# Performance work log

Hardware: AMD Instinct MI355X
Metric: run time of the kernel (lower is better)

The kernel has to match this reference:

```python
import jax, jax.numpy as jnp
import numpy as np

H = 16  # num_heads
THETA = 10000.0


def apply_rope(x, positions, theta=THETA):
    # x: [..., S, d_k]; positions: [S]
    d_k = x.shape[-1]
    inv_freq = theta ** (-jnp.arange(0, d_k, 2, dtype=jnp.float32) / d_k)  # [d_k/2]
    ang = positions.astype(jnp.float32)[:, None] * inv_freq[None, :]  # [S, d_k/2]
    cos, sin = jnp.cos(ang), jnp.sin(ang)
    x1 = x[..., 0::2]
    x2 = x[..., 1::2]
    out_even = x1 * cos - x2 * sin
    out_odd = x1 * sin + x2 * cos
    out = jnp.stack([out_even, out_odd], axis=-1)  # [..., S, d_k/2, 2]
    return out.reshape(x.shape)


def setup_inputs() -> dict:
    key = jax.random.key(0)
    k1, k2, k3 = jax.random.split(key, 3)
    B, S, D = 2, 2048, 1024
    x = jax.random.normal(k1, (B, S, D), dtype=jnp.float32)
    token_positions = jnp.arange(S, dtype=jnp.int32)
    w_qkv = jax.random.normal(k2, (3 * D, D), dtype=jnp.float32) * (D ** -0.5)
    w_out = jax.random.normal(k3, (D, D), dtype=jnp.float32) * (D ** -0.5)
    return {"x": x, "token_positions": token_positions, "w_qkv": w_qkv, "w_out": w_out}


def reference(x, token_positions, w_qkv, w_out):
    B, S, D = x.shape
    d_k = D // H
    qkv = jnp.einsum('bsd,ed->bse', x, w_qkv)  # [B,S,3D]
    # split '(n h d_k)' -> n=3, h=H, d_k
    qkv = qkv.reshape(B, S, 3, H, d_k).transpose(2, 0, 3, 1, 4)  # [3,B,H,S,d_k]
    q = apply_rope(qkv[0], token_positions)
    k = apply_rope(qkv[1], token_positions)
    v = qkv[2]
    scale = 1.0 / jnp.sqrt(jnp.asarray(d_k, dtype=x.dtype))
    scores = jnp.einsum('bhqd,bhkd->bhqk', q, k) * scale  # [B,H,S,S]
    causal = jnp.tril(jnp.ones((S, S), dtype=bool))
    scores = jnp.where(causal, scores, jnp.asarray(-1e30, dtype=scores.dtype))
    attn = jax.nn.softmax(scores, axis=-1)
    out = jnp.einsum('bhqk,bhkd->bhqd', attn, v)  # [B,H,S,d_k]
    out = out.transpose(0, 2, 1, 3).reshape(B, S, D)  # merge (h d_v)
    return jnp.einsum('bsd,ed->bse', out, w_out)
```

## Files before the change

### kernel.cpp

```cpp
#include <hip/hip_runtime.h>

using bf16 = __bf16;
typedef __bf16 bf16x2 __attribute__((ext_vector_type(2)));
typedef __bf16 bf16x4v __attribute__((ext_vector_type(4)));
typedef __bf16 bf16x8 __attribute__((ext_vector_type(8)));
typedef float f32x4 __attribute__((ext_vector_type(4)));
typedef float floatx4 __attribute__((ext_vector_type(4)));

#define MFMA16(a, b, c) __builtin_amdgcn_mfma_f32_16x16x32_bf16((a), (b), (c), 0, 0, 0)

__device__ __forceinline__ float exp2a(float x) {
  float r;
  asm("v_exp_f32 %0, %1" : "=v"(r) : "v"(x));
  return r;
}

__global__ __launch_bounds__(256) void cast3_kernel(const float* __restrict__ a,
                                                    const float* __restrict__ b,
                                                    const float* __restrict__ c,
                                                    bf16* __restrict__ oa,
                                                    bf16* __restrict__ ob,
                                                    bf16* __restrict__ oc,
                                                    const int* __restrict__ pos,
                                                    float2* __restrict__ tab) {
  int i = blockIdx.x * 256 + threadIdx.x;
  if (i < 65536) {
    int s = i >> 5, ip = i & 31;
    float freq = exp2f(-(float)ip * (13.287712379549449f / 32.0f));
    float ang = (float)pos[s] * freq;
    float sn, cs;
    sincosf(ang, &sn, &cs);
    tab[i] = make_float2(cs, sn);
  }
  const float* in;
  bf16* out;
  int off;
  if (i < 1048576) {
    in = a; out = oa; off = i;
  } else if (i < 1835008) {
    in = b; out = ob; off = i - 1048576;
  } else {
    in = c; out = oc; off = i - 1835008;
  }
  floatx4 v = *(const floatx4*)(in + (size_t)off * 4);
  bf16x4v o;
  #pragma unroll
  for (int j = 0; j < 4; ++j) o[j] = (bf16)v[j];
  *(bf16x4v*)(out + (size_t)off * 4) = o;
}

template <bool OUT_F32, bool ROPE>
__global__ __launch_bounds__(256, 2) void gemm_bt(const bf16* __restrict__ A,
                                                  const bf16* __restrict__ B,
                                                  void* __restrict__ Cv,
                                                  int M, int N, int K,
                                                  const float2* __restrict__ tab) {
  __shared__ bf16 As[128 * 32];
  __shared__ bf16 Bs[128 * 32];
  const int t = threadIdx.x;
  const int l = t & 63;
  const int w = t >> 6;
  const int m0 = blockIdx.y * 128;
  const int n0 = blockIdx.x * 128;
  const int wr = (w >> 1) * 64;
  const int wc = (w & 1) * 64;
  const int lr = l & 15;
  const int lk = (l >> 4) * 8;

  f32x4 acc[4][4] = {};

  const int srow = t >> 2;
  const int scol = (t & 3) * 8;

  for (int k0 = 0; k0 < K; k0 += 32) {
    __syncthreads();
    #pragma unroll
    for (int j = 0; j < 2; ++j) {
      const bf16* ga = A + (size_t)(m0 + j * 64 + srow) * K + k0 + scol;
      __builtin_amdgcn_global_load_lds(
          (const __attribute__((address_space(1))) void*)ga,
          (__attribute__((address_space(3))) void*)(As + (j * 64 + srow) * 32 + scol),
          16, 0, 0);
      const bf16* gb = B + (size_t)(n0 + j * 64 + srow) * K + k0 + scol;
      __builtin_amdgcn_global_load_lds(
          (const __attribute__((address_space(1))) void*)gb,
          (__attribute__((address_space(3))) void*)(Bs + (j * 64 + srow) * 32 + scol),
          16, 0, 0);
    }
    __syncthreads();
    bf16x8 af[4], bfr[4];
    #pragma unroll
    for (int i = 0; i < 4; ++i) af[i] = *(const bf16x8*)(As + (wr + i * 16 + lr) * 32 + lk);
    #pragma unroll
    for (int i = 0; i < 4; ++i) bfr[i] = *(const bf16x8*)(Bs + (wc + i * 16 + lr) * 32 + lk);
    #pragma unroll
    for (int i = 0; i < 4; ++i)
      #pragma unroll
      for (int j = 0; j < 4; ++j)
        acc[i][j] = MFMA16(af[i], bfr[j], acc[i][j]);
  }

  const int cr0 = (l >> 4) * 4;
  const int cc = l & 15;

  if constexpr (ROPE) {
    if (n0 < 2048) {
      int ip[4];
      #pragma unroll
      for (int j = 0; j < 4; ++j) ip[j] = ((n0 + wc + j * 16 + cc) & 63) >> 1;
      const float sgn = (cc & 1) ? 1.f : -1.f;
      #pragma unroll
      for (int i = 0; i < 4; ++i) {
        #pragma unroll
        for (int r = 0; r < 4; ++r) {
          int row = m0 + wr + i * 16 + cr0 + r;
          int s = row & 2047;
          #pragma unroll
          for (int j = 0; j < 4; ++j) {
            float2 cs = tab[s * 32 + ip[j]];
            float self = acc[i][j][r];
            float partner = __shfl_xor(self, 1, 64);
            acc[i][j][r] = self * cs.x + sgn * cs.y * partner;
          }
        }
      }
    }
  }

  #pragma unroll
  for (int i = 0; i < 4; ++i) {
    #pragma unroll
    for (int j = 0; j < 4; ++j) {
      int row = m0 + wr + i * 16 + cr0;
      int col = n0 + wc + j * 16 + cc;
      #pragma unroll
      for (int r = 0; r < 4; ++r) {
        if constexpr (OUT_F32)
          ((float*)Cv)[(size_t)(row + r) * N + col] = acc[i][j][r];
        else
          ((bf16*)Cv)[(size_t)(row + r) * N + col] = (bf16)acc[i][j][r];
      }
    }
  }
}

__global__ __launch_bounds__(512, 4) void fa_causal(const bf16* __restrict__ qkv,
                                                    bf16* __restrict__ attn) {
  const int bh = blockIdx.x;
  const int b = bh >> 4, h = bh & 15;
  const int q0 = ((int)gridDim.y - 1 - (int)blockIdx.y) * 128;
  const int t = threadIdx.x, w = t >> 6, l = t & 63;
  const int lq = l & 15;
  const int g = l >> 4;
  const int lk = g * 8;
  const int swz = lq & 7;
  const int hz = lq >> 3;

  __shared__ bf16 SH[4][64 * 64];

  const size_t rs = 3072;
  const bf16* Qg = qkv + (size_t)(b * 2048) * rs + h * 64;
  const bf16* Kg = Qg + 1024;
  const bf16* Vg = Qg + 2048;

  const int qrow0 = q0 + w * 16;
  const int qg = qrow0 + lq;

  const float SC = 0.125f * 1.44269504088896f;
  bf16x8 qfr[2];
  #pragma unroll
  for (int kk = 0; kk < 2; ++kk) {
    bf16x8 qv = *(const bf16x8*)(Qg + (size_t)qg * rs + kk * 32 + lk);
    #pragma unroll
    for (int j = 0; j < 8; ++j) qv[j] = (bf16)((float)qv[j] * SC);
    qfr[kk] = qv;
  }

  f32x4 o[4] = {};
  float mrow = -1e30f, lrow = 0.f;

  const int nkt = (q0 + 128) >> 6;
  const int krow_in = l >> 3;
  const int kcsrc = (l & 7) ^ krow_in;
  const int kp = t >> 4;
  const int K0 = kp * 2;
  const int sub = (t >> 3) & 1;
  const int cd = t & 7;
  const int slot0 = (K0 & 32) | (((K0 >> 2) & 3) << 3) | (((K0 >> 4) & 1) << 2) | (K0 & 3);

  bf16x4v va4, vb4;

  #define STAGE_K(KT, BUF)                                                              \
    {                                                                                   \
      const bf16* src = Kg + (size_t)((KT)*64 + w * 8 + krow_in) * rs + kcsrc * 8;      \
      __builtin_amdgcn_global_load_lds(                                                 \
          (const __attribute__((address_space(1))) void*)src,                           \
          (__attribute__((address_space(3))) void*)(&SH[BUF][(w * 8) * 64]), 16, 0, 0); \
    }
  #define LOAD_V(KT)                                                                   \
    {                                                                                  \
      const bf16* vsrc = Vg + (size_t)((KT)*64 + K0) * rs + cd * 8 + sub * 4;          \
      va4 = *(const bf16x4v*)(vsrc);                                                   \
      vb4 = *(const bf16x4v*)(vsrc + rs);                                              \
    }
  #define WRITE_V(BUF)                                                                 \
    {                                                                                  \
      _Pragma("unroll")                                                                \
      for (int j = 0; j < 4; ++j) {                                                    \
        int e = sub * 4 + j;                                                           \
        bf16x2 pr;                                                                     \
        pr[0] = va4[j];                                                                \
        pr[1] = vb4[j];                                                                \
        *(bf16x2*)(&SH[2 + (BUF)][(cd * 8 + e) * 64 + (slot0 ^ ((e ^ cd) << 3))]) = pr; \
      }                                                                                \
    }

  STAGE_K(0, 0)
  LOAD_V(0)
  WRITE_V(0)
  __syncthreads();

  for (int kt = 0; kt < nkt; ++kt) {
    const bool pf = (kt + 1 < nkt);
    if (pf) {
      LOAD_V(kt + 1)
      STAGE_K(kt + 1, (kt + 1) & 1)
    }

    if (kt * 64 <= qrow0 + 15) {
      const bf16* Kc = SH[kt & 1];
      const bf16* Vc = SH[2 + (kt & 1)];
      const bool fullw = (kt * 64 + 63 <= qrow0);

      f32x4 sc[4] = {};
      __builtin_amdgcn_s_setprio(1);
      #pragma unroll
      for (int kf = 0; kf < 4; ++kf) {
        const int krow = kf * 16 + lq;
        bf16x8 kb0 = *(const bf16x8*)(&Kc[krow * 64 + ((0 + g) ^ swz) * 8]);
        bf16x8 kb1 = *(const bf16x8*)(&Kc[krow * 64 + ((4 + g) ^ swz) * 8]);
        sc[kf] = MFMA16(kb0, qfr[0], sc[kf]);
        sc[kf] = MFMA16(kb1, qfr[1], sc[kf]);
      }
      __builtin_amdgcn_s_setprio(0);

      float pv[16];
      if (fullw) {
        #pragma unroll
        for (int i = 0; i < 16; ++i) pv[i] = sc[i >> 2][i & 3];
      } else {
        #pragma unroll
        for (int kf = 0; kf < 4; ++kf)
          #pragma unroll
          for (int r = 0; r < 4; ++r) {
            int key = kt * 64 + kf * 16 + g * 4 + r;
            pv[kf * 4 + r] = (key <= qg) ? sc[kf][r] : -1e30f;
          }
      }
      float m0_ = fmaxf(pv[0], pv[1]), m1_ = fmaxf(pv[2], pv[3]);
      float m2_ = fmaxf(pv[4], pv[5]), m3_ = fmaxf(pv[6], pv[7]);
      float m4_ = fmaxf(pv[8], pv[9]), m5_ = fmaxf(pv[10], pv[11]);
      float m6_ = fmaxf(pv[12], pv[13]), m7_ = fmaxf(pv[14], pv[15]);
      float ma = fmaxf(fmaxf(m0_, m1_), fmaxf(m2_, m3_));
      float mb = fmaxf(fmaxf(m4_, m5_), fmaxf(m6_, m7_));
      float mxl = fmaxf(ma, mb);
      if (!__all(mxl <= mrow)) {
        float mx = fmaxf(mxl, __shfl_xor(mxl, 16, 64));
        mx = fmaxf(mx, __shfl_xor(mx, 32, 64));
        float mnew = fmaxf(mrow, mx);
        float al = exp2a(mrow - mnew);
        lrow *= al;
        #pragma unroll
        for (int fd = 0; fd < 4; ++fd)
          #pragma unroll
          for (int r = 0; r < 4; ++r) o[fd][r] *= al;
        mrow = mnew;
      }
      #pragma unroll
      for (int i = 0; i < 16; ++i) pv[i] = exp2a(pv[i] - mrow);
      float s0_ = pv[0] + pv[1], s1_ = pv[2] + pv[3];
      float s2_ = pv[4] + pv[5], s3_ = pv[6] + pv[7];
      float s4_ = pv[8] + pv[9], s5_ = pv[10] + pv[11];
      float s6_ = pv[12] + pv[13], s7_ = pv[14] + pv[15];
      float rsum = ((s0_ + s1_) + (s2_ + s3_)) + ((s4_ + s5_) + (s6_ + s7_));
      rsum += __shfl_xor(rsum, 16, 64);
      rsum += __shfl_xor(rsum, 32, 64);
      lrow += rsum;

      bf16x8 p0, p1;
      #pragma unroll
      for (int i = 0; i < 8; ++i) {
        p0[i] = (bf16)pv[i];
        p1[i] = (bf16)pv[8 + i];
      }

      __builtin_amdgcn_s_setprio(1);
      #pragma unroll
      for (int fd = 0; fd < 4; ++fd) {
        const int drow = fd * 16 + lq;
        {
          int pc = (0 * 4 + g) ^ swz ^ (fd << 1) ^ hz;
          bf16x8 vb = *(const bf16x8*)(&Vc[drow * 64 + pc * 8]);
          o[fd] = MFMA16(vb, p0, o[fd]);
        }
        {
          int pc = (1 * 4 + g) ^ swz ^ (fd << 1) ^ hz;
          bf16x8 vb = *(const bf16x8*)(&Vc[drow * 64 + pc * 8]);
          o[fd] = MFMA16(vb, p1, o[fd]);
        }
      }
      __builtin_amdgcn_s_setprio(0);
    }

    if (pf) {
      WRITE_V((kt + 1) & 1)
      __syncthreads();
    }
  }

  __syncthreads();
  bf16* Os = (bf16*)SH + w * (16 * 72);
  float inv = 1.0f / lrow;
  #pragma unroll
  for (int fd = 0; fd < 4; ++fd) {
    bf16x4v ov;
    #pragma unroll
    for (int r = 0; r < 4; ++r) ov[r] = (bf16)(o[fd][r] * inv);
    *(bf16x4v*)(&Os[lq * 72 + fd * 16 + g * 4]) = ov;
  }
  asm volatile("" ::: "memory");
  #pragma unroll
  for (int p = 0; p < 2; ++p) {
    int idx = p * 64 + l;
    int row16 = idx >> 3, c8 = idx & 7;
    bf16x8 v = *(const bf16x8*)(&Os[row16 * 72 + c8 * 8]);
    *(bf16x8*)(&attn[(size_t)(b * 2048 + qrow0 + row16) * 1024 + h * 64 + c8 * 8]) = v;
  }
}

extern "C" void kernel_launch(void* const* d_in, const int* in_sizes, int n_in,
                              void* d_out, int out_size, void* d_ws, size_t ws_size,
                              hipStream_t stream) {
  const float* x = (const float*)d_in[0];
  const int* pos = (const int*)d_in[1];
  const float* w_qkv = (const float*)d_in[2];
  const float* w_out = (const float*)d_in[3];
  float* out = (float*)d_out;

  char* ws = (char*)d_ws;
  bf16* xb   = (bf16*)(ws);
  bf16* wqb  = (bf16*)(ws + (8u << 20));
  bf16* wob  = (bf16*)(ws + (14u << 20));
  bf16* qkv  = (bf16*)(ws + (16u << 20));
  bf16* attn = (bf16*)(ws + (40u << 20));
  float2* tab = (float2*)(ws + (40u << 20));

  cast3_kernel<<<8192, 256, 0, stream>>>(x, w_qkv, w_out, xb, wqb, wob, pos, tab);

  dim3 g1(3072 / 128, 4096 / 128);
  gemm_bt<false, true><<<g1, 256, 0, stream>>>(xb, wqb, (void*)qkv, 4096, 3072, 1024, tab);

  dim3 gfa(32, 2048 / 128);
  fa_causal<<<gfa, 512, 0, stream>>>(qkv, attn);

  dim3 g2(1024 / 128, 4096 / 128);
  gemm_bt<true, false><<<g2, 256, 0, stream>>>(attn, wob, (void*)out, 4096, 1024, 1024, nullptr);
}
```

Before: 115.0 us.

## Pair short and long causal query tiles per block for balanced flash attention

Flash attention blocks shrink from 512 threads over 128 query rows to 256 threads over 64 rows. Each block now handles two 64-row query tiles in sequence, tile y and tile 31-y, so every block does about the same amount of causal work. K/V staging is changed so 4 waves load the whole 64-row tile, each thread moving more data. This aims to remove tail imbalance from the causal triangle, at the cost of less parallelism per block and more K/V reloads, since a 64-row query tile shares less data.

```diff
diff --git a/kernel.cpp b/kernel.cpp
--- a/kernel.cpp
+++ b/kernel.cpp
@@ -144,11 +144,10 @@
   }
 }
 
-__global__ __launch_bounds__(512, 4) void fa_causal(const bf16* __restrict__ qkv,
+__global__ __launch_bounds__(256, 4) void fa_causal(const bf16* __restrict__ qkv,
                                                     bf16* __restrict__ attn) {
   const int bh = blockIdx.x;
   const int b = bh >> 4, h = bh & 15;
-  const int q0 = ((int)gridDim.y - 1 - (int)blockIdx.y) * 128;
   const int t = threadIdx.x, w = t >> 6, l = t & 63;
   const int lq = l & 15;
   const int g = l >> 4;
@@ -156,185 +155,196 @@
   const int swz = lq & 7;
   const int hz = lq >> 3;
 
-  __shared__ bf16 SH[4][64 * 64];
+  __shared__ bf16 Ks[2][64 * 64];
+  __shared__ bf16 Vt[2][64 * 64];
 
   const size_t rs = 3072;
   const bf16* Qg = qkv + (size_t)(b * 2048) * rs + h * 64;
   const bf16* Kg = Qg + 1024;
   const bf16* Vg = Qg + 2048;
 
-  const int qrow0 = q0 + w * 16;
-  const int qg = qrow0 + lq;
-
   const float SC = 0.125f * 1.44269504088896f;
-  bf16x8 qfr[2];
-  #pragma unroll
-  for (int kk = 0; kk < 2; ++kk) {
-    bf16x8 qv = *(const bf16x8*)(Qg + (size_t)qg * rs + kk * 32 + lk);
-    #pragma unroll
-    for (int j = 0; j < 8; ++j) qv[j] = (bf16)((float)qv[j] * SC);
-    qfr[kk] = qv;
-  }
-
-  f32x4 o[4] = {};
-  float mrow = -1e30f, lrow = 0.f;
-
-  const int nkt = (q0 + 128) >> 6;
+
   const int krow_in = l >> 3;
   const int kcsrc = (l & 7) ^ krow_in;
-  const int kp = t >> 4;
+  const int kp = t >> 3;
   const int K0 = kp * 2;
-  const int sub = (t >> 3) & 1;
   const int cd = t & 7;
   const int slot0 = (K0 & 32) | (((K0 >> 2) & 3) << 3) | (((K0 >> 4) & 1) << 2) | (K0 & 3);
 
-  bf16x4v va4, vb4;
-
-  #define STAGE_K(KT, BUF)                                                              \
-    {                                                                                   \
-      const bf16* src = Kg + (size_t)((KT)*64 + w * 8 + krow_in) * rs + kcsrc * 8;      \
-      __builtin_amdgcn_global_load_lds(                                                 \
-          (const __attribute__((address_space(1))) void*)src,                           \
-          (__attribute__((address_space(3))) void*)(&SH[BUF][(w * 8) * 64]), 16, 0, 0); \
-    }
-  #define LOAD_V(KT)                                                                   \
-    {                                                                                  \
-      const bf16* vsrc = Vg + (size_t)((KT)*64 + K0) * rs + cd * 8 + sub * 4;          \
-      va4 = *(const bf16x4v*)(vsrc);                                                   \
-      vb4 = *(const bf16x4v*)(vsrc + rs);                                              \
-    }
-  #define WRITE_V(BUF)                                                                 \
-    {                                                                                  \
-      _Pragma("unroll")                                                                \
-      for (int j = 0; j < 4; ++j) {                                                    \
-        int e = sub * 4 + j;                                                           \
-        bf16x2 pr;                                                                     \
-        pr[0] = va4[j];                                                                \
-        pr[1] = vb4[j];                                                                \
-        *(bf16x2*)(&SH[2 + (BUF)][(cd * 8 + e) * 64 + (slot0 ^ ((e ^ cd) << 3))]) = pr; \
-      }                                                                                \
-    }
-
-  STAGE_K(0, 0)
-  LOAD_V(0)
-  WRITE_V(0)
-  __syncthreads();
-
-  for (int kt = 0; kt < nkt; ++kt) {
-    const bool pf = (kt + 1 < nkt);
-    if (pf) {
-      LOAD_V(kt + 1)
-      STAGE_K(kt + 1, (kt + 1) & 1)
-    }
-
-    if (kt * 64 <= qrow0 + 15) {
-      const bf16* Kc = SH[kt & 1];
-      const bf16* Vc = SH[2 + (kt & 1)];
-      const bool fullw = (kt * 64 + 63 <= qrow0);
-
-      f32x4 sc[4] = {};
-      __builtin_amdgcn_s_setprio(1);
-      #pragma unroll
-      for (int kf = 0; kf < 4; ++kf) {
-        const int krow = kf * 16 + lq;
-        bf16x8 kb0 = *(const bf16x8*)(&Kc[krow * 64 + ((0 + g) ^ swz) * 8]);
-        bf16x8 kb1 = *(const bf16x8*)(&Kc[krow * 64 + ((4 + g) ^ swz) * 8]);
-        sc[kf] = MFMA16(kb0, qfr[0], sc[kf]);
-        sc[kf] = MFMA16(kb1, qfr[1], sc[kf]);
-      }
-      __builtin_amdgcn_s_setprio(0);
-
-      float pv[16];
-      if (fullw) {
-        #pragma unroll
-        for (int i = 0; i < 16; ++i) pv[i] = sc[i >> 2][i & 3];
-      } else {
-        #pragma unroll
-        for (int kf = 0; kf < 4; ++kf)
+  bf16x8 va, vb2;
+
+  #define STAGE_K(KT, BUF)                                                                \
+    {                                                                                     \
+      _Pragma("unroll")                                                                   \
+      for (int c = 0; c < 2; ++c) {                                                       \
+        const int rowbase = w * 8 + c * 32;                                               \
+        const bf16* src = Kg + (size_t)((KT)*64 + rowbase + krow_in) * rs + kcsrc * 8;    \
+        __builtin_amdgcn_global_load_lds(                                                 \
+            (const __attribute__((address_space(1))) void*)src,                           \
+            (__attribute__((address_space(3))) void*)(&Ks[BUF][rowbase * 64]), 16, 0, 0); \
+      }                                                                                   \
+    }
+  #define LOAD_V(KT)                                                          \
+    {                                                                         \
+      const bf16* vsrc = Vg + (size_t)((KT)*64 + K0) * rs + cd * 8;           \
+      va = *(const bf16x8*)(vsrc);                                            \
+      vb2 = *(const bf16x8*)(vsrc + rs);                                      \
+    }
+  #define WRITE_V(BUF)                                                        \
+    {                                                                         \
+      _Pragma("unroll")                                                       \
+      for (int e = 0; e < 8; ++e) {                                           \
+        bf16x2 pr;                                                            \
+        pr[0] = va[e];                                                        \
+        pr[1] = vb2[e];                                                       \
+        *(bf16x2*)(&Vt[BUF][(cd * 8 + e) * 64 + (slot0 ^ ((e ^ cd) << 3))]) = pr; \
+      }                                                                       \
+    }
+
+  #pragma unroll 1
+  for (int seg = 0; seg < 2; ++seg) {
+    const int qt = seg ? (31 - (int)blockIdx.y) : (int)blockIdx.y;
+    const int q0 = qt * 64;
+    const int qrow0 = q0 + w * 16;
+    const int qg = qrow0 + lq;
+    const int nkt = qt + 1;
+
+    bf16x8 qfr[2];
+    #pragma unroll
+    for (int kk = 0; kk < 2; ++kk) {
+      bf16x8 qv = *(const bf16x8*)(Qg + (size_t)qg * rs + kk * 32 + lk);
+      #pragma unroll
+      for (int j = 0; j < 8; ++j) qv[j] = (bf16)((float)qv[j] * SC);
+      qfr[kk] = qv;
+    }
+
+    f32x4 o[4] = {};
+    float mrow = -1e30f, lrow = 0.f;
+
+    if (seg) __syncthreads();
+
+    STAGE_K(0, 0)
+    LOAD_V(0)
+    WRITE_V(0)
+    __syncthreads();
+
+    for (int kt = 0; kt < nkt; ++kt) {
+      const bool pf = (kt + 1 < nkt);
+      if (pf) {
+        LOAD_V(kt + 1)
+        STAGE_K(kt + 1, (kt + 1) & 1)
+      }
+
+      if (kt * 64 <= qrow0 + 15) {
+        const bf16* Kc = Ks[kt & 1];
+        const bf16* Vc = Vt[kt & 1];
+        const bool fullw = (kt * 64 + 63 <= qrow0);
+
+        f32x4 sc[4] = {};
+        __builtin_amdgcn_s_setprio(1);
+        #pragma unroll
+        for (int kf = 0; kf < 4; ++kf) {
+          const int krow = kf * 16 + lq;
+          bf16x8 kb0 = *(const bf16x8*)(&Kc[krow * 64 + ((0 + g) ^ swz) * 8]);
+          bf16x8 kb1 = *(const bf16x8*)(&Kc[krow * 64 + ((4 + g) ^ swz) * 8]);
+          sc[kf] = MFMA16(kb0, qfr[0], sc[kf]);
+          sc[kf] = MFMA16(kb1, qfr[1], sc[kf]);
+        }
+        __builtin_amdgcn_s_setprio(0);
+
+        float pv[16];
+        if (fullw) {
           #pragma unroll
-          for (int r = 0; r < 4; ++r) {
-            int key = kt * 64 + kf * 16 + g * 4 + r;
-            pv[kf * 4 + r] = (key <= qg) ? sc[kf][r] : -1e30f;
+          for (int i = 0; i < 16; ++i) pv[i] = sc[i >> 2][i & 3];
+        } else {
+          #pragma unroll
+          for (int kf = 0; kf < 4; ++kf)
+            #pragma unroll
+            for (int r = 0; r < 4; ++r) {
+              int key = kt * 64 + kf * 16 + g * 4 + r;
+              pv[kf * 4 + r] = (key <= qg) ? sc[kf][r] : -1e30f;
+            }
+        }
+        float m0_ = fmaxf(pv[0], pv[1]), m1_ = fmaxf(pv[2], pv[3]);
+        float m2_ = fmaxf(pv[4], pv[5]), m3_ = fmaxf(pv[6], pv[7]);
+        float m4_ = fmaxf(pv[8], pv[9]), m5_ = fmaxf(pv[10], pv[11]);
+        float m6_ = fmaxf(pv[12], pv[13]), m7_ = fmaxf(pv[14], pv[15]);
+        float ma = fmaxf(fmaxf(m0_, m1_), fmaxf(m2_, m3_));
+        float mb = fmaxf(fmaxf(m4_, m5_), fmaxf(m6_, m7_));
+        float mxl = fmaxf(ma, mb);
+        if (!__all(mxl <= mrow)) {
+          float mx = fmaxf(mxl, __shfl_xor(mxl, 16, 64));
+          mx = fmaxf(mx, __shfl_xor(mx, 32, 64));
+          float mnew = fmaxf(mrow, mx);
+          float al = exp2a(mrow - mnew);
+          lrow *= al;
+          #pragma unroll
+          for (int fd = 0; fd < 4; ++fd)
+            #pragma unroll
+            for (int r = 0; r < 4; ++r) o[fd][r] *= al;
+          mrow = mnew;
+        }
+        #pragma unroll
+        for (int i = 0; i < 16; ++i) pv[i] = exp2a(pv[i] - mrow);
+        float s0_ = pv[0] + pv[1], s1_ = pv[2] + pv[3];
+        float s2_ = pv[4] + pv[5], s3_ = pv[6] + pv[7];
+        float s4_ = pv[8] + pv[9], s5_ = pv[10] + pv[11];
+        float s6_ = pv[12] + pv[13], s7_ = pv[14] + pv[15];
+        float rsum = ((s0_ + s1_) + (s2_ + s3_)) + ((s4_ + s5_) + (s6_ + s7_));
+        rsum += __shfl_xor(rsum, 16, 64);
+        rsum += __shfl_xor(rsum, 32, 64);
+        lrow += rsum;
+
+        bf16x8 p0, p1;
+        #pragma unroll
+        for (int i = 0; i < 8; ++i) {
+          p0[i] = (bf16)pv[i];
+          p1[i] = (bf16)pv[8 + i];
+        }
+
+        __builtin_amdgcn_s_setprio(1);
+        #pragma unroll
+        for (int fd = 0; fd < 4; ++fd) {
+          const int drow = fd * 16 + lq;
+          {
+            int pc = (0 * 4 + g) ^ swz ^ (fd << 1) ^ hz;
+            bf16x8 vb = *(const bf16x8*)(&Vc[drow * 64 + pc * 8]);
+            o[fd] = MFMA16(vb, p0, o[fd]);
           }
-      }
-      float m0_ = fmaxf(pv[0], pv[1]), m1_ = fmaxf(pv[2], pv[3]);
-      float m2_ = fmaxf(pv[4], pv[5]), m3_ = fmaxf(pv[6], pv[7]);
-      float m4_ = fmaxf(pv[8], pv[9]), m5_ = fmaxf(pv[10], pv[11]);
-      float m6_ = fmaxf(pv[12], pv[13]), m7_ = fmaxf(pv[14], pv[15]);
-      float ma = fmaxf(fmaxf(m0_, m1_), fmaxf(m2_, m3_));
-      float mb = fmaxf(fmaxf(m4_, m5_), fmaxf(m6_, m7_));
-      float mxl = fmaxf(ma, mb);
-      if (!__all(mxl <= mrow)) {
-        float mx = fmaxf(mxl, __shfl_xor(mxl, 16, 64));
-        mx = fmaxf(mx, __shfl_xor(mx, 32, 64));
-        float mnew = fmaxf(mrow, mx);
-        float al = exp2a(mrow - mnew);
-        lrow *= al;
-        #pragma unroll
-        for (int fd = 0; fd < 4; ++fd)
-          #pragma unroll
-          for (int r = 0; r < 4; ++r) o[fd][r] *= al;
-        mrow = mnew;
-      }
-      #pragma unroll
-      for (int i = 0; i < 16; ++i) pv[i] = exp2a(pv[i] - mrow);
-      float s0_ = pv[0] + pv[1], s1_ = pv[2] + pv[3];
-      float s2_ = pv[4] + pv[5], s3_ = pv[6] + pv[7];
-      float s4_ = pv[8] + pv[9], s5_ = pv[10] + pv[11];
-      float s6_ = pv[12] + pv[13], s7_ = pv[14] + pv[15];
-      float rsum = ((s0_ + s1_) + (s2_ + s3_)) + ((s4_ + s5_) + (s6_ + s7_));
-      rsum += __shfl_xor(rsum, 16, 64);
-      rsum += __shfl_xor(rsum, 32, 64);
-      lrow += rsum;
-
-      bf16x8 p0, p1;
-      #pragma unroll
-      for (int i = 0; i < 8; ++i) {
-        p0[i] = (bf16)pv[i];
-        p1[i] = (bf16)pv[8 + i];
-      }
-
-      __builtin_amdgcn_s_setprio(1);
-      #pragma unroll
-      for (int fd = 0; fd < 4; ++fd) {
-        const int drow = fd * 16 + lq;
-        {
-          int pc = (0 * 4 + g) ^ swz ^ (fd << 1) ^ hz;
-          bf16x8 vb = *(const bf16x8*)(&Vc[drow * 64 + pc * 8]);
-          o[fd] = MFMA16(vb, p0, o[fd]);
-        }
-        {
-          int pc = (1 * 4 + g) ^ swz ^ (fd << 1) ^ hz;
-          bf16x8 vb = *(const bf16x8*)(&Vc[drow * 64 + pc * 8]);
-          o[fd] = MFMA16(vb, p1, o[fd]);
-        }
-      }
-      __builtin_amdgcn_s_setprio(0);
-    }
-
-    if (pf) {
-      WRITE_V((kt + 1) & 1)
-      __syncthreads();
-    }
-  }
-
-  __syncthreads();
-  bf16* Os = (bf16*)SH + w * (16 * 72);
-  float inv = 1.0f / lrow;
-  #pragma unroll
-  for (int fd = 0; fd < 4; ++fd) {
-    bf16x4v ov;
-    #pragma unroll
-    for (int r = 0; r < 4; ++r) ov[r] = (bf16)(o[fd][r] * inv);
-    *(bf16x4v*)(&Os[lq * 72 + fd * 16 + g * 4]) = ov;
-  }
-  asm volatile("" ::: "memory");
-  #pragma unroll
-  for (int p = 0; p < 2; ++p) {
-    int idx = p * 64 + l;
-    int row16 = idx >> 3, c8 = idx & 7;
-    bf16x8 v = *(const bf16x8*)(&Os[row16 * 72 + c8 * 8]);
-    *(bf16x8*)(&attn[(size_t)(b * 2048 + qrow0 + row16) * 1024 + h * 64 + c8 * 8]) = v;
+          {
+            int pc = (1 * 4 + g) ^ swz ^ (fd << 1) ^ hz;
+            bf16x8 vb = *(const bf16x8*)(&Vc[drow * 64 + pc * 8]);
+            o[fd] = MFMA16(vb, p1, o[fd]);
+          }
+        }
+        __builtin_amdgcn_s_setprio(0);
+      }
+
+      if (pf) {
+        WRITE_V((kt + 1) & 1)
+        __syncthreads();
+      }
+    }
+
+    __syncthreads();
+    bf16* Os = (bf16*)Ks + w * (16 * 72);
+    float inv = 1.0f / lrow;
+    #pragma unroll
+    for (int fd = 0; fd < 4; ++fd) {
+      bf16x4v ov;
+      #pragma unroll
+      for (int r = 0; r < 4; ++r) ov[r] = (bf16)(o[fd][r] * inv);
+      *(bf16x4v*)(&Os[lq * 72 + fd * 16 + g * 4]) = ov;
+    }
+    asm volatile("" ::: "memory");
+    #pragma unroll
+    for (int p = 0; p < 2; ++p) {
+      int idx = p * 64 + l;
+      int row16 = idx >> 3, c8 = idx & 7;
+      bf16x8 v = *(const bf16x8*)(&Os[row16 * 72 + c8 * 8]);
+      *(bf16x8*)(&attn[(size_t)(b * 2048 + qrow0 + row16) * 1024 + h * 64 + c8 * 8]) = v;
+    }
   }
 }
 
@@ -360,8 +370,8 @@
   dim3 g1(3072 / 128, 4096 / 128);
   gemm_bt<false, true><<<g1, 256, 0, stream>>>(xb, wqb, (void*)qkv, 4096, 3072, 1024, tab);
 
-  dim3 gfa(32, 2048 / 128);
-  fa_causal<<<gfa, 512, 0, stream>>>(qkv, attn);
+  dim3 gfa(32, 16);
+  fa_causal<<<gfa, 256, 0, stream>>>(qkv, attn);
 
   dim3 g2(1024 / 128, 4096 / 128);
   gemm_bt<true, false><<<g2, 256, 0, stream>>>(attn, wob, (void*)out, 4096, 1024, 1024, nullptr);
```

After: 118.8 us. 3.3% more time.
